# Optimization experiments

Hardware: AMD Instinct MI355X
Metric: run time of the kernel (lower is better)

Reference implementation:

```python
import jax, jax.numpy as jnp
import numpy as np

LEVELS = 3  # num_basis = 1 + 1 + 2 + 4 = 8


def _haar_basis(x):
    """Closed-form vectorized Haar basis, x: [B, F] raw inputs.

    Replaces the original nested per-feature/per-level/per-bucket mask loops:
    at each level only one bucket k = floor(u*freq) is active, with value
    +2^(level/2) on the left half of the bucket and -2^(level/2) on the right
    half (x == 1.0 falls in the right half of the last bucket, matching the
    torch edge-case handling).
    """
    u = (jnp.tanh(x) + 1.0) / 2.0  # normalize to [0, 1]
    cols = [jnp.ones_like(u)[..., None]]  # scaling function phi
    for level in range(LEVELS):
        freq = 2 ** level
        k = jnp.clip(jnp.floor(u * freq), 0, freq - 1).astype(jnp.int32)  # bucket idx
        mid = (k.astype(u.dtype) + 0.5) / freq
        amp = jnp.asarray(2.0 ** (level / 2), u.dtype)
        sign = jnp.where(u < mid, amp, -amp)  # [B, F]
        cols.append(jax.nn.one_hot(k, freq, dtype=u.dtype) * sign[..., None])
    return jnp.concatenate(cols, axis=-1)  # [B, F, num_basis]


def setup_inputs() -> dict:
    key = jax.random.key(0)
    k1, k2, k3 = jax.random.split(key, 3)
    B, F, O, NB = 32768, 1024, 64, 8
    x = jax.random.normal(k1, (B, F), dtype=jnp.float32)
    coeffs = jax.random.normal(k2, (F, O, NB), dtype=jnp.float32) * 0.05
    base_weight = jax.random.normal(k3, (F, O), dtype=jnp.float32) * 0.05
    return {"x": x, "coeffs": coeffs, "base_weight": base_weight}


def reference(x, coeffs, base_weight):
    basis = _haar_basis(x)                         # [B, F, NB]
    wave_out = jnp.einsum('bin,ion->bo', basis, coeffs)  # [B, O]
    out = wave_out + x @ base_weight               # residual path
    kl = jnp.zeros((1,), dtype=x.dtype)            # non-variational: kl = 0
    return (out, kl)
```

## Files before the change

kernel.cpp:

```cpp
#include <hip/hip_runtime.h>
#include <math.h>
#include <string.h>


typedef __attribute__((ext_vector_type(8))) short short8;
typedef __attribute__((ext_vector_type(4))) float f32x4;

__device__ __forceinline__ unsigned int f2bf(float f) {
  unsigned int u = __float_as_uint(f);
  u += 0x7FFFu + ((u >> 16) & 1u);
  return u >> 16;
}

__device__ __forceinline__ void gen_basis(int j, unsigned int* d) {
  d[0] = (j < 4) ? 0x3F803F80u : 0xBF803F80u;
  unsigned int sq1 = (j & 2) ? 0xBFB5u : 0x3FB5u;
  d[1] = (j & 4) ? (sq1 << 16) : sq1;
  unsigned long long sd2 = (j & 1) ? 0xC000ull : 0x4000ull;
  unsigned long long d23 = sd2 << ((j & 6) << 3);
  d[2] = (unsigned int)d23;
  d[3] = (unsigned int)(d23 >> 32);
}

#define BARRIER() __asm__ volatile("s_waitcnt lgkmcnt(0)\n\ts_barrier" ::: "memory")

__global__ __launch_bounds__(256) void build_w(const float* __restrict__ coeffs,
                                               const float* __restrict__ bw,
                                               uint4* __restrict__ Wsw) {
  const int l = threadIdx.x & 63;
  const int t = threadIdx.x >> 6;
  const int g = blockIdx.x;
  const int c = g / 9, j = g - c * 9;
  const int R = c * 4 + (l >> 4);
  const int o = t * 16 + (l & 15);
  unsigned int dwv[4];
#pragma unroll
  for (int jj = 0; jj < 8; ++jj) {
    int d = 8 * j + jj;
    int p = d / 18;
    int e = d - p * 18;
    int f, n;
    if (e < 8)       { f = 8 * R + 2 * p;     n = e; }
    else if (e == 8) { f = 8 * R + 2 * p;     n = 8; }
    else if (e == 9) { f = 8 * R + 2 * p + 1; n = 8; }
    else             { f = 8 * R + 2 * p + 1; n = e - 10; }
    float v = (n < 8) ? coeffs[(f * 64 + o) * 8 + n] : bw[f * 64 + o];
    unsigned int h = f2bf(v);
    if (jj & 1) dwv[jj >> 1] |= h << 16; else dwv[jj >> 1] = h;
  }
  uint4 qq; qq.x = dwv[0]; qq.y = dwv[1]; qq.z = dwv[2]; qq.w = dwv[3];
  Wsw[(g * 4 + t) * 64 + l] = qq;
}

__global__ __launch_bounds__(256, 4) void wavelet_gemm(const float* __restrict__ x,
                                                       const uint4* __restrict__ Wsw,
                                                       float* __restrict__ out,
                                                       int out_size,
                                                       float4 Ta, float4 Tb) {
  __shared__ uint4 Albuf[18 * 4 * 32];
  const int tid = threadIdx.x;
  const int l = tid & 63;
  const int w = tid >> 6;
  const int q = l >> 4;
  const int mm = l & 15;
  const int m = tid & 31;
  const int r = tid >> 5;
  const long rowbase = (long)blockIdx.x * 32;

  f32x4 acc[8];
#pragma unroll
  for (int i = 0; i < 8; ++i) acc[i] = (f32x4){0.f, 0.f, 0.f, 0.f};

  const float* xrow = x + (rowbase + m) * 1024 + r * 8;
  const int wboff = ((r >> 2) * 36 + (r & 3)) * 32 + m;

  float4 xa = *(const float4*)(xrow);
  float4 xb = *(const float4*)(xrow + 4);

  for (int sc = 0; sc < 16; ++sc) {
    float xv[8];
    xv[0] = xa.x; xv[1] = xa.y; xv[2] = xa.z; xv[3] = xa.w;
    xv[4] = xb.x; xv[5] = xb.y; xv[6] = xb.z; xv[7] = xb.w;
    unsigned int dw[36];
#pragma unroll
    for (int p = 0; p < 4; ++p) {
      float xe = xv[2 * p], xo = xv[2 * p + 1];
      int je = (xe >= Ta.x) + (xe >= Ta.y) + (xe >= Ta.z) + (xe >= Ta.w)
             + (xe >= Tb.x) + (xe >= Tb.y) + (xe >= Tb.z);
      int jo = (xo >= Ta.x) + (xo >= Ta.y) + (xo >= Ta.z) + (xo >= Ta.w)
             + (xo >= Tb.x) + (xo >= Tb.y) + (xo >= Tb.z);
      gen_basis(je, &dw[9 * p]);
      dw[9 * p + 4] = f2bf(xe) | (f2bf(xo) << 16);
      gen_basis(jo, &dw[9 * p + 5]);
    }
#pragma unroll
    for (int gg = 0; gg < 9; ++gg) {
      uint4 qv; qv.x = dw[4 * gg]; qv.y = dw[4 * gg + 1];
      qv.z = dw[4 * gg + 2]; qv.w = dw[4 * gg + 3];
      Albuf[wboff + gg * 128] = qv;
    }
    BARRIER();
    if (sc + 1 < 16) {
      xa = *(const float4*)(xrow + (sc + 1) * 64);
      xb = *(const float4*)(xrow + (sc + 1) * 64 + 4);
    }
    const int t = w ^ ((sc & 1) << 1);
    const int NS = (t < 2) ? 5 : 4;
    for (int i = 0; i < NS; ++i) {
      const int s = t + 4 * i;
      const uint4* ab = Albuf + (s * 4 + q) * 32 + mm;
      short8 a0 = __builtin_bit_cast(short8, ab[0]);
      short8 a1 = __builtin_bit_cast(short8, ab[16]);
      const uint4* wp = Wsw + (size_t)(sc * 18 + s) * 256 + l;
      short8 b0 = __builtin_bit_cast(short8, wp[0]);
      short8 b1 = __builtin_bit_cast(short8, wp[64]);
      short8 b2 = __builtin_bit_cast(short8, wp[128]);
      short8 b3 = __builtin_bit_cast(short8, wp[192]);
      acc[0] = __builtin_amdgcn_mfma_f32_16x16x32_bf16(a0, b0, acc[0], 0, 0, 0);
      acc[1] = __builtin_amdgcn_mfma_f32_16x16x32_bf16(a0, b1, acc[1], 0, 0, 0);
      acc[2] = __builtin_amdgcn_mfma_f32_16x16x32_bf16(a0, b2, acc[2], 0, 0, 0);
      acc[3] = __builtin_amdgcn_mfma_f32_16x16x32_bf16(a0, b3, acc[3], 0, 0, 0);
      acc[4] = __builtin_amdgcn_mfma_f32_16x16x32_bf16(a1, b0, acc[4], 0, 0, 0);
      acc[5] = __builtin_amdgcn_mfma_f32_16x16x32_bf16(a1, b1, acc[5], 0, 0, 0);
      acc[6] = __builtin_amdgcn_mfma_f32_16x16x32_bf16(a1, b2, acc[6], 0, 0, 0);
      acc[7] = __builtin_amdgcn_mfma_f32_16x16x32_bf16(a1, b3, acc[7], 0, 0, 0);
    }
    BARRIER();
  }

  float* P = (float*)Albuf;
#pragma unroll
  for (int s = 0; s < 8; ++s)
    *(f32x4*)(P + w * 2048 + s * 256 + 4 * l) = acc[s];
  BARRIER();
  float* og = out + (size_t)rowbase * 64;
#pragma unroll
  for (int si = 0; si < 2; ++si) {
    const int s = 2 * w + si;
    f32x4 v = *(f32x4*)(P + 0 * 2048 + s * 256 + 4 * l);
    v = v + *(f32x4*)(P + 1 * 2048 + s * 256 + 4 * l);
    v = v + *(f32x4*)(P + 2 * 2048 + s * 256 + 4 * l);
    v = v + *(f32x4*)(P + 3 * 2048 + s * 256 + 4 * l);
    const int rt = s >> 2, tt = s & 3;
#pragma unroll
    for (int e = 0; e < 4; ++e)
      og[(16 * rt + 4 * q + e) * 64 + 16 * tt + mm] = v[e];
  }
  if (blockIdx.x == 0 && tid == 0) out[out_size - 1] = 0.0f;
}

static unsigned int f32key(float f) {
  unsigned int u; memcpy(&u, &f, 4);
  return (u & 0x80000000u) ? ~u : (u | 0x80000000u);
}
static float f32unkey(unsigned int k) {
  unsigned int u = (k & 0x80000000u) ? (k ^ 0x80000000u) : ~k;
  float f; memcpy(&f, &u, 4);
  return f;
}
static bool pipe_ge(float x, int k) {
  float tf = (float)tanh((double)x);
  float s = (tf + 1.0f) * 0.5f;
  float t8 = s * 8.0f;
  return t8 >= (float)k;
}
static void thresholds(float* X) {
  for (int k = 1; k <= 7; ++k) {
    unsigned int lo = f32key(-4.0f);
    unsigned int hi = f32key(4.0f);
    while (hi - lo > 1) {
      unsigned int mid = lo + (hi - lo) / 2;
      if (pipe_ge(f32unkey(mid), k)) hi = mid; else lo = mid;
    }
    X[k - 1] = f32unkey(hi);
  }
}

extern "C" void kernel_launch(void* const* d_in, const int* in_sizes, int n_in,
                              void* d_out, int out_size, void* d_ws, size_t ws_size,
                              hipStream_t stream) {
  const float* x      = (const float*)d_in[0];
  const float* coeffs = (const float*)d_in[1];
  const float* bw     = (const float*)d_in[2];
  uint4* Wsw = (uint4*)d_ws;
  float* out = (float*)d_out;

  float X[7];
  thresholds(X);
  float4 Ta; Ta.x = X[0]; Ta.y = X[1]; Ta.z = X[2]; Ta.w = X[3];
  float4 Tb; Tb.x = X[4]; Tb.y = X[5]; Tb.z = X[6]; Tb.w = 1e30f;

  build_w<<<288, 256, 0, stream>>>(coeffs, bw, Wsw);
  wavelet_gemm<<<1024, 256, 0, stream>>>(x, (const uint4*)Wsw, out, out_size, Ta, Tb);
}
```

Measured before the change: 248.8 us.

## Double row tile to 64 per block and restructure K-chunk distribution across waves

Each block now handles 64 rows instead of 32, with 16 accumulators per wave, so every weight fragment loaded from global memory feeds twice as many MFMAs. The K loop is split into 32 chunks of 32 features (9 k-steps each), rotated across waves. The LDS reduction epilogue now runs in two halves. This halves the grid to 512 blocks and raises register pressure, which may cut occupancy and cause load imbalance, since wave t==0 does an extra step.

```diff
diff --git a/kernel.cpp b/kernel.cpp
--- a/kernel.cpp
+++ b/kernel.cpp
@@ -52,32 +52,65 @@
   Wsw[(g * 4 + t) * 64 + l] = qq;
 }
 
+__device__ __forceinline__ void mfma_step(const uint4* __restrict__ Albuf,
+                                          const uint4* __restrict__ Wsw,
+                                          f32x4* acc, int g, int s,
+                                          int q, int mm, int l) {
+  const uint4* wp = Wsw + (size_t)g * 256 + l;
+  uint4 b0 = wp[0], b1 = wp[64], b2 = wp[128], b3 = wp[192];
+  const uint4* ab = Albuf + (s * 4 + q) * 64 + mm;
+  short8 a0 = __builtin_bit_cast(short8, ab[0]);
+  short8 a1 = __builtin_bit_cast(short8, ab[16]);
+  short8 a2 = __builtin_bit_cast(short8, ab[32]);
+  short8 a3 = __builtin_bit_cast(short8, ab[48]);
+  short8 B0 = __builtin_bit_cast(short8, b0);
+  short8 B1 = __builtin_bit_cast(short8, b1);
+  short8 B2 = __builtin_bit_cast(short8, b2);
+  short8 B3 = __builtin_bit_cast(short8, b3);
+  acc[0]  = __builtin_amdgcn_mfma_f32_16x16x32_bf16(a0, B0, acc[0],  0, 0, 0);
+  acc[1]  = __builtin_amdgcn_mfma_f32_16x16x32_bf16(a0, B1, acc[1],  0, 0, 0);
+  acc[2]  = __builtin_amdgcn_mfma_f32_16x16x32_bf16(a0, B2, acc[2],  0, 0, 0);
+  acc[3]  = __builtin_amdgcn_mfma_f32_16x16x32_bf16(a0, B3, acc[3],  0, 0, 0);
+  acc[4]  = __builtin_amdgcn_mfma_f32_16x16x32_bf16(a1, B0, acc[4],  0, 0, 0);
+  acc[5]  = __builtin_amdgcn_mfma_f32_16x16x32_bf16(a1, B1, acc[5],  0, 0, 0);
+  acc[6]  = __builtin_amdgcn_mfma_f32_16x16x32_bf16(a1, B2, acc[6],  0, 0, 0);
+  acc[7]  = __builtin_amdgcn_mfma_f32_16x16x32_bf16(a1, B3, acc[7],  0, 0, 0);
+  acc[8]  = __builtin_amdgcn_mfma_f32_16x16x32_bf16(a2, B0, acc[8],  0, 0, 0);
+  acc[9]  = __builtin_amdgcn_mfma_f32_16x16x32_bf16(a2, B1, acc[9],  0, 0, 0);
+  acc[10] = __builtin_amdgcn_mfma_f32_16x16x32_bf16(a2, B2, acc[10], 0, 0, 0);
+  acc[11] = __builtin_amdgcn_mfma_f32_16x16x32_bf16(a2, B3, acc[11], 0, 0, 0);
+  acc[12] = __builtin_amdgcn_mfma_f32_16x16x32_bf16(a3, B0, acc[12], 0, 0, 0);
+  acc[13] = __builtin_amdgcn_mfma_f32_16x16x32_bf16(a3, B1, acc[13], 0, 0, 0);
+  acc[14] = __builtin_amdgcn_mfma_f32_16x16x32_bf16(a3, B2, acc[14], 0, 0, 0);
+  acc[15] = __builtin_amdgcn_mfma_f32_16x16x32_bf16(a3, B3, acc[15], 0, 0, 0);
+}
+
 __global__ __launch_bounds__(256, 4) void wavelet_gemm(const float* __restrict__ x,
                                                        const uint4* __restrict__ Wsw,
                                                        float* __restrict__ out,
                                                        int out_size,
                                                        float4 Ta, float4 Tb) {
-  __shared__ uint4 Albuf[18 * 4 * 32];
+  __shared__ uint4 Albuf[9 * 4 * 64];
   const int tid = threadIdx.x;
   const int l = tid & 63;
   const int w = tid >> 6;
   const int q = l >> 4;
   const int mm = l & 15;
-  const int m = tid & 31;
-  const int r = tid >> 5;
-  const long rowbase = (long)blockIdx.x * 32;
-
-  f32x4 acc[8];
-#pragma unroll
-  for (int i = 0; i < 8; ++i) acc[i] = (f32x4){0.f, 0.f, 0.f, 0.f};
+  const int m = tid & 63;
+  const int r = tid >> 6;
+  const long rowbase = (long)blockIdx.x * 64;
+
+  f32x4 acc[16];
+#pragma unroll
+  for (int i = 0; i < 16; ++i) acc[i] = (f32x4){0.f, 0.f, 0.f, 0.f};
 
   const float* xrow = x + (rowbase + m) * 1024 + r * 8;
-  const int wboff = ((r >> 2) * 36 + (r & 3)) * 32 + m;
+  const int wboff = r * 64 + m;
 
   float4 xa = *(const float4*)(xrow);
   float4 xb = *(const float4*)(xrow + 4);
 
-  for (int sc = 0; sc < 16; ++sc) {
+  for (int c = 0; c < 32; ++c) {
     float xv[8];
     xv[0] = xa.x; xv[1] = xa.y; xv[2] = xa.z; xv[3] = xa.w;
     xv[4] = xb.x; xv[5] = xb.y; xv[6] = xb.z; xv[7] = xb.w;
@@ -97,54 +130,42 @@
     for (int gg = 0; gg < 9; ++gg) {
       uint4 qv; qv.x = dw[4 * gg]; qv.y = dw[4 * gg + 1];
       qv.z = dw[4 * gg + 2]; qv.w = dw[4 * gg + 3];
-      Albuf[wboff + gg * 128] = qv;
-    }
-    BARRIER();
-    if (sc + 1 < 16) {
-      xa = *(const float4*)(xrow + (sc + 1) * 64);
-      xb = *(const float4*)(xrow + (sc + 1) * 64 + 4);
-    }
-    const int t = w ^ ((sc & 1) << 1);
-    const int NS = (t < 2) ? 5 : 4;
-    for (int i = 0; i < NS; ++i) {
-      const int s = t + 4 * i;
-      const uint4* ab = Albuf + (s * 4 + q) * 32 + mm;
-      short8 a0 = __builtin_bit_cast(short8, ab[0]);
-      short8 a1 = __builtin_bit_cast(short8, ab[16]);
-      const uint4* wp = Wsw + (size_t)(sc * 18 + s) * 256 + l;
-      short8 b0 = __builtin_bit_cast(short8, wp[0]);
-      short8 b1 = __builtin_bit_cast(short8, wp[64]);
-      short8 b2 = __builtin_bit_cast(short8, wp[128]);
-      short8 b3 = __builtin_bit_cast(short8, wp[192]);
-      acc[0] = __builtin_amdgcn_mfma_f32_16x16x32_bf16(a0, b0, acc[0], 0, 0, 0);
-      acc[1] = __builtin_amdgcn_mfma_f32_16x16x32_bf16(a0, b1, acc[1], 0, 0, 0);
-      acc[2] = __builtin_amdgcn_mfma_f32_16x16x32_bf16(a0, b2, acc[2], 0, 0, 0);
-      acc[3] = __builtin_amdgcn_mfma_f32_16x16x32_bf16(a0, b3, acc[3], 0, 0, 0);
-      acc[4] = __builtin_amdgcn_mfma_f32_16x16x32_bf16(a1, b0, acc[4], 0, 0, 0);
-      acc[5] = __builtin_amdgcn_mfma_f32_16x16x32_bf16(a1, b1, acc[5], 0, 0, 0);
-      acc[6] = __builtin_amdgcn_mfma_f32_16x16x32_bf16(a1, b2, acc[6], 0, 0, 0);
-      acc[7] = __builtin_amdgcn_mfma_f32_16x16x32_bf16(a1, b3, acc[7], 0, 0, 0);
-    }
+      Albuf[wboff + gg * 256] = qv;
+    }
+    BARRIER();
+    if (c + 1 < 32) {
+      xa = *(const float4*)(xrow + (c + 1) * 32);
+      xb = *(const float4*)(xrow + (c + 1) * 32 + 4);
+    }
+    const int t = (w + c) & 3;
+    mfma_step(Albuf, Wsw, acc, c * 9 + t,     t,     q, mm, l);
+    mfma_step(Albuf, Wsw, acc, c * 9 + t + 4, t + 4, q, mm, l);
+    if (t == 0)
+      mfma_step(Albuf, Wsw, acc, c * 9 + 8,   8,     q, mm, l);
     BARRIER();
   }
 
   float* P = (float*)Albuf;
-#pragma unroll
-  for (int s = 0; s < 8; ++s)
-    *(f32x4*)(P + w * 2048 + s * 256 + 4 * l) = acc[s];
-  BARRIER();
   float* og = out + (size_t)rowbase * 64;
 #pragma unroll
-  for (int si = 0; si < 2; ++si) {
-    const int s = 2 * w + si;
-    f32x4 v = *(f32x4*)(P + 0 * 2048 + s * 256 + 4 * l);
-    v = v + *(f32x4*)(P + 1 * 2048 + s * 256 + 4 * l);
-    v = v + *(f32x4*)(P + 2 * 2048 + s * 256 + 4 * l);
-    v = v + *(f32x4*)(P + 3 * 2048 + s * 256 + 4 * l);
-    const int rt = s >> 2, tt = s & 3;
-#pragma unroll
-    for (int e = 0; e < 4; ++e)
-      og[(16 * rt + 4 * q + e) * 64 + 16 * tt + mm] = v[e];
+  for (int h = 0; h < 2; ++h) {
+#pragma unroll
+    for (int s = 0; s < 8; ++s)
+      *(f32x4*)(P + w * 2048 + s * 256 + 4 * l) = acc[8 * h + s];
+    BARRIER();
+#pragma unroll
+    for (int si = 0; si < 2; ++si) {
+      const int s = 2 * w + si;
+      f32x4 v = *(f32x4*)(P + 0 * 2048 + s * 256 + 4 * l);
+      v = v + *(f32x4*)(P + 1 * 2048 + s * 256 + 4 * l);
+      v = v + *(f32x4*)(P + 2 * 2048 + s * 256 + 4 * l);
+      v = v + *(f32x4*)(P + 3 * 2048 + s * 256 + 4 * l);
+      const int sg = 8 * h + s, rt = sg >> 2, tt = sg & 3;
+#pragma unroll
+      for (int e = 0; e < 4; ++e)
+        og[(16 * rt + 4 * q + e) * 64 + 16 * tt + mm] = v[e];
+    }
+    BARRIER();
   }
   if (blockIdx.x == 0 && tid == 0) out[out_size - 1] = 0.0f;
 }
@@ -191,5 +212,5 @@
   float4 Tb; Tb.x = X[4]; Tb.y = X[5]; Tb.z = X[6]; Tb.w = 1e30f;
 
   build_w<<<288, 256, 0, stream>>>(coeffs, bw, Wsw);
-  wavelet_gemm<<<1024, 256, 0, stream>>>(x, (const uint4*)Wsw, out, out_size, Ta, Tb);
-}
+  wavelet_gemm<<<512, 256, 0, stream>>>(x, (const uint4*)Wsw, out, out_size, Ta, Tb);
+}
```

New measurement: 250.5 us. No clear change (+0.7%).
